# Optimization experiments

Measured on AMD Instinct MI355X. Metric: run time of the kernel, lower is better.

## Reference

```python
import jax, jax.numpy as jnp
import numpy as np
from jax import lax

N = 100_000          # points
NEIGH = 16           # max_num_neighbors
E = N * NEIGH        # edges
DIN = 128            # num_inputs
D2 = 64              # bottleneck dim = num_outputs // 4
DOUT = 256           # num_outputs
K = 15               # num_kernel_points
SIGMA = 0.04         # kernel_influence_dist = prev_grid_size * sigma
NEG = 0.1            # LeakyReLU slope
EPS = 1e-5           # BatchNorm eps


def leaky(x):
    return jnp.where(x >= 0, x, NEG * x)


def batchnorm(x, g, b):
    # training-mode BN over the point dimension (biased variance, like torch)
    m = jnp.mean(x, axis=0)
    v = jnp.var(x, axis=0)
    return (x - m) * (g / jnp.sqrt(v + EPS)) + b


def setup_inputs() -> dict:
    key = jax.random.key(0)
    ks = jax.random.split(key, 12)
    pos = jax.random.uniform(ks[0], (N, 4), dtype=jnp.float32) * 0.1  # col 0: batch idx (unused, non-strided)
    x = jax.random.normal(ks[1], (N, DIN), dtype=jnp.float32)
    e_ref = jax.random.randint(ks[2], (E,), 0, N)
    e_query = jax.random.randint(ks[3], (E,), 0, N)
    # fixed kernel point positions within the influence radius
    kernel_points = jax.random.normal(ks[4], (K, 3), dtype=jnp.float32) * (0.5 * SIGMA)
    W1 = jax.random.normal(ks[5], (DIN, D2), dtype=jnp.float32) / np.sqrt(DIN)
    W_kp = jax.random.normal(ks[6], (K, D2, D2), dtype=jnp.float32) / np.sqrt(D2 * K)
    W2 = jax.random.normal(ks[7], (D2, DOUT), dtype=jnp.float32) / np.sqrt(D2)
    Wsc = jax.random.normal(ks[8], (DIN, DOUT), dtype=jnp.float32) / np.sqrt(DIN)
    ones = lambda d: jnp.ones((d,), jnp.float32)
    zeros = lambda d: jnp.zeros((d,), jnp.float32)
    return dict(pos=pos, x=x, e_ref=e_ref, e_query=e_query,
                W1=W1, g1=ones(D2), b1=zeros(D2),
                kernel_points=kernel_points, W_kp=W_kp, gkp=ones(D2), bkp=zeros(D2),
                W2=W2, g2=ones(DOUT), b2=zeros(DOUT),
                Wsc=Wsc, gsc=ones(DOUT), bsc=zeros(DOUT))


def reference(pos, x, e_ref, e_query, W1, g1, b1, kernel_points, W_kp, gkp, bkp,
              W2, g2, b2, Wsc, gsc, bsc):
    n = x.shape[0]
    # bottleneck unary_1: Linear(no bias) -> BN -> LeakyReLU
    h = leaky(batchnorm(x @ W1, g1, b1))                      # [N, D2]
    # KPConv (rigid, linear influence, 'sum' aggregation); non-strided: query_pos == pos
    rel = pos[e_ref, 1:] - pos[e_query, 1:]                    # [E, 3]
    d2 = jnp.sum((rel[:, None, :] - kernel_points[None]) ** 2, axis=-1)  # [E, K]
    infl = jnp.maximum(0.0, 1.0 - jnp.sqrt(d2) / SIGMA)        # [E, K]
    feat_e = h[e_ref]                                          # [E, D2] neighbor gather

    def body(acc, inp):
        infl_k, Wk = inp                                       # [E], [D2, D2]
        agg = jax.ops.segment_sum(infl_k[:, None] * feat_e, e_query, num_segments=n)
        return acc + agg @ Wk, None

    y0 = jnp.zeros((n, W_kp.shape[-1]), x.dtype)
    y, _ = lax.scan(body, y0, (infl.T, W_kp))                  # [N, D2]
    # SimpleBlock post: BN -> LeakyReLU
    y = leaky(batchnorm(y, gkp, bkp))
    # bottleneck unary_2: Linear -> BN -> LeakyReLU
    y = leaky(batchnorm(y @ W2, g2, b2))
    # shortcut (num_inputs != num_outputs): Linear -> BN, no activation; residual add
    skip = batchnorm(x @ Wsc, gsc, bsc)
    return y + skip
```

## Files before the change

### kernel.cpp

```cpp
#include <hip/hip_runtime.h>
#include <math.h>

#define NP   100000
#define EDG  1600000
#define NK   15
#define SIGK 0.04f
#define SCH  2048
#define SNB  49
#define MAXE 256
#define AGP  968
#define ISTR 20

typedef __bf16 v8bf __attribute__((ext_vector_type(8)));
typedef __bf16 bf4  __attribute__((ext_vector_type(4)));
typedef float  v4f  __attribute__((ext_vector_type(4)));

__device__ __forceinline__ float lk(float v) { return v >= 0.f ? v : 0.1f * v; }
__device__ __forceinline__ float bf2f(__bf16 b) { return (float)b; }

template <int KIN, int NB, bool TRANS, bool OUTBF>
__global__ __launch_bounds__(256) void mgemm_k(const float* __restrict__ X,
                                               const __bf16* __restrict__ Wp,
                                               void* __restrict__ Out, int n, int Ntot,
                                               const float* __restrict__ ta,
                                               const float* __restrict__ tb,
                                               float* __restrict__ osum,
                                               float* __restrict__ osq) {
  constexpr int PITCH = KIN + 8;
  constexpr int NT = NB / 16;
  __shared__ __bf16 al[128 * PITCH];
  __shared__ float red[2][NB][4];
  const int tid = threadIdx.x;
  const int r0 = blockIdx.x << 7;
  const int nb0 = blockIdx.y * NB;

  constexpr int QKS = (KIN == 128) ? 5 : 4;
  for (int idx = tid; idx < (128 << QKS); idx += 256) {
    const int r = idx >> QKS, q = (idx & ((1 << QKS) - 1)) << 2;
    const int row = r0 + r;
    float4 v = make_float4(0.f, 0.f, 0.f, 0.f);
    if (row < n) {
      v = *(const float4*)&X[(size_t)row * KIN + q];
      if (TRANS) {
        v.x = lk(ta[q + 0] * v.x + tb[q + 0]);
        v.y = lk(ta[q + 1] * v.y + tb[q + 1]);
        v.z = lk(ta[q + 2] * v.z + tb[q + 2]);
        v.w = lk(ta[q + 3] * v.w + tb[q + 3]);
      }
    }
    bf4 o;
    o[0] = (__bf16)v.x; o[1] = (__bf16)v.y; o[2] = (__bf16)v.z; o[3] = (__bf16)v.w;
    *(bf4*)&al[r * PITCH + q] = o;
  }
  __syncthreads();

  const int wv = tid >> 6, lane = tid & 63;
  const int mr = lane & 15, quad = lane >> 4;
  const int ntg0 = nb0 >> 4;
  const int NTG = Ntot >> 4;
  v4f acc[2][NT];
#pragma unroll
  for (int a = 0; a < 2; ++a)
#pragma unroll
    for (int b = 0; b < NT; ++b) acc[a][b] = (v4f){0.f, 0.f, 0.f, 0.f};

#pragma unroll
  for (int ks = 0; ks < KIN / 32; ++ks) {
    v8bf bf[NT];
#pragma unroll
    for (int nt = 0; nt < NT; ++nt)
      bf[nt] = ((const v8bf*)Wp)[((size_t)ks * NTG + ntg0 + nt) * 64 + lane];
#pragma unroll
    for (int mt = 0; mt < 2; ++mt) {
      const int row = (wv << 5) + (mt << 4) + mr;
      const v8bf av = *(const v8bf*)&al[row * PITCH + (ks << 5) + (quad << 3)];
#pragma unroll
      for (int nt = 0; nt < NT; ++nt)
        acc[mt][nt] = __builtin_amdgcn_mfma_f32_16x16x32_bf16(av, bf[nt], acc[mt][nt], 0, 0, 0);
    }
  }

  float csum[NT], csq[NT];
#pragma unroll
  for (int nt = 0; nt < NT; ++nt) { csum[nt] = 0.f; csq[nt] = 0.f; }
#pragma unroll
  for (int mt = 0; mt < 2; ++mt)
#pragma unroll
    for (int nt = 0; nt < NT; ++nt)
#pragma unroll
      for (int r = 0; r < 4; ++r) {
        const float v = acc[mt][nt][r];
        const int row = r0 + (wv << 5) + (mt << 4) + (quad << 2) + r;
        if (row < n) {
          const size_t o = (size_t)row * Ntot + nb0 + (nt << 4) + mr;
          if (OUTBF) ((__bf16*)Out)[o] = (__bf16)v;
          else       ((float*)Out)[o] = v;
        }
        csum[nt] += v;
        csq[nt] += v * v;
      }
#pragma unroll
  for (int nt = 0; nt < NT; ++nt) {
    float s = csum[nt], q = csq[nt];
    s += __shfl_down(s, 32); s += __shfl_down(s, 16);
    q += __shfl_down(q, 32); q += __shfl_down(q, 16);
    if (quad == 0) { red[0][(nt << 4) + mr][wv] = s; red[1][(nt << 4) + mr][wv] = q; }
  }
  __syncthreads();
  if (tid < NB) {
    const float s = red[0][tid][0] + red[0][tid][1] + red[0][tid][2] + red[0][tid][3];
    const float q = red[1][tid][0] + red[1][tid][1] + red[1][tid][2] + red[1][tid][3];
    const int rep = (blockIdx.x & 31) * Ntot;
    atomicAdd(&osum[rep + nb0 + tid], s);
    atomicAdd(&osq[rep + nb0 + tid], q);
  }
}

__global__ void finalize_k(const float* __restrict__ sum, const float* __restrict__ sq,
                           const float* __restrict__ g, const float* __restrict__ b,
                           float* __restrict__ oa, float* __restrict__ ob, int C, int R,
                           float invn) {
  const int c = threadIdx.x;
  if (c < C) {
    float s = 0.f, q = 0.f;
    for (int r = 0; r < R; ++r) { s += sum[r * C + c]; q += sq[r * C + c]; }
    const float m = s * invn;
    const float var = q * invn - m * m;
    const float a = g[c] / sqrtf(var + 1e-5f);
    oa[c] = a;
    ob[c] = b[c] - m * a;
  }
}

__global__ __launch_bounds__(256) void final_k(float* __restrict__ o,
                                               const __bf16* __restrict__ t2,
                                               const __bf16* __restrict__ tsc,
                                               const float* __restrict__ a2,
                                               const float* __restrict__ b2,
                                               const float* __restrict__ asc,
                                               const float* __restrict__ bsc) {
  const int idx = (blockIdx.x << 8) + threadIdx.x;
  const int c = (idx << 2) & 255;
  const bf4 tv = *(const bf4*)&t2[(size_t)idx << 2];
  const bf4 sv = *(const bf4*)&tsc[(size_t)idx << 2];
  float4 r;
  r.x = lk(a2[c + 0] * bf2f(tv[0]) + b2[c + 0]) + asc[c + 0] * bf2f(sv[0]) + bsc[c + 0];
  r.y = lk(a2[c + 1] * bf2f(tv[1]) + b2[c + 1]) + asc[c + 1] * bf2f(sv[1]) + bsc[c + 1];
  r.z = lk(a2[c + 2] * bf2f(tv[2]) + b2[c + 2]) + asc[c + 2] * bf2f(sv[2]) + bsc[c + 2];
  r.w = lk(a2[c + 3] * bf2f(tv[3]) + b2[c + 3]) + asc[c + 3] * bf2f(sv[3]) + bsc[c + 3];
  ((float4*)o)[idx] = r;
}

__device__ __forceinline__ bool edge_active(const float* __restrict__ pos,
                                            const float* __restrict__ kp,
                                            int ref, int q) {
  const float4 pr = *(const float4*)&pos[ref * 4];
  const float4 pq = *(const float4*)&pos[q * 4];
  const float rx = pr.y - pq.y, ry = pr.z - pq.z, rz = pr.w - pq.w;
  bool act = false;
#pragma unroll
  for (int k = 0; k < NK; ++k) {
    const float dx = rx - kp[k * 3 + 0];
    const float dy = ry - kp[k * 3 + 1];
    const float dz = rz - kp[k * 3 + 2];
    act = act || (dx * dx + dy * dy + dz * dz < SIGK * SIGK);
  }
  return act;
}

__global__ __launch_bounds__(256) void hist_k(const int* __restrict__ er,
                                              const int* __restrict__ eq,
                                              const float* __restrict__ pos,
                                              const float* __restrict__ kp,
                                              int* __restrict__ cnt,
                                              unsigned char* __restrict__ flags) {
  const int stride = gridDim.x << 8;
  for (int e = (blockIdx.x << 8) + threadIdx.x; e < EDG; e += stride) {
    const int q = eq[e];
    const bool act = edge_active(pos, kp, er[e], q);
    flags[e] = act ? 1 : 0;
    if (act) atomicAdd(&cnt[q], 1);
  }
}

__global__ __launch_bounds__(256) void scanA_k(const int* __restrict__ cnt, int* __restrict__ part) {
  __shared__ int s[256];
  const int tid = threadIdx.x;
  const int base = blockIdx.x * SCH;
  int acc = 0;
  for (int i = tid; i < SCH; i += 256) {
    const int idx = base + i;
    if (idx < NP) acc += cnt[idx];
  }
  s[tid] = acc;
  __syncthreads();
  for (int d = 128; d > 0; d >>= 1) {
    if (tid < d) s[tid] += s[tid + d];
    __syncthreads();
  }
  if (tid == 0) part[blockIdx.x] = s[0];
}

__global__ void scanB_k(int* __restrict__ part, int* __restrict__ off) {
  if (threadIdx.x == 0) {
    int run = 0;
    for (int i = 0; i < SNB; ++i) { const int v = part[i]; part[i] = run; run += v; }
    off[NP] = run;
  }
}

__global__ __launch_bounds__(256) void scanC_k(const int* __restrict__ cnt,
                                               const int* __restrict__ part,
                                               int* __restrict__ off, int* __restrict__ cur) {
  __shared__ int s[256];
  const int tid = threadIdx.x;
  const int base = blockIdx.x * SCH + tid * 8;
  int loc[8];
  int mysum = 0;
#pragma unroll
  for (int j = 0; j < 8; ++j) {
    const int idx = base + j;
    const int v = (idx < NP) ? cnt[idx] : 0;
    loc[j] = mysum;
    mysum += v;
  }
  s[tid] = mysum;
  __syncthreads();
  for (int d = 1; d < 256; d <<= 1) {
    int v = (tid >= d) ? s[tid - d] : 0;
    __syncthreads();
    s[tid] += v;
    __syncthreads();
  }
  const int tb = part[blockIdx.x] + s[tid] - mysum;
#pragma unroll
  for (int j = 0; j < 8; ++j) {
    const int idx = base + j;
    if (idx < NP) { off[idx] = tb + loc[j]; cur[idx] = tb + loc[j]; }
  }
}

__global__ __launch_bounds__(256) void scat_k(const int* __restrict__ er,
                                              const int* __restrict__ eq,
                                              const unsigned char* __restrict__ flags,
                                              int* __restrict__ cur, int* __restrict__ sref) {
  const int stride = gridDim.x << 8;
  for (int e = (blockIdx.x << 8) + threadIdx.x; e < EDG; e += stride) {
    if (flags[e]) {
      const int p = atomicAdd(&cur[eq[e]], 1);
      if (p < EDG) sref[p] = er[e];
    }
  }
}

__device__ __forceinline__ void wshuf1(const float* W, __bf16* Wp, int idx, int Ntot) {
  const int j = idx & 7;
  const int lane = (idx >> 3) & 63;
  const int rest = idx >> 9;
  const int NTG = Ntot >> 4;
  const int ntg = rest % NTG;
  const int ks = rest / NTG;
  Wp[idx] = (__bf16)W[(size_t)(ks * 32 + ((lane >> 4) << 3) + j) * Ntot + ntg * 16 + (lane & 15)];
}

__global__ __launch_bounds__(256) void allshuf_k(const float* __restrict__ W1,
                                                 const float* __restrict__ Wsc,
                                                 const float* __restrict__ W2,
                                                 const float* __restrict__ Wkp,
                                                 __bf16* __restrict__ base) {
  const int i = (blockIdx.x << 8) + threadIdx.x;
  if (i < 8192) {
    wshuf1(W1, base, i, 64);
  } else if (i < 40960) {
    wshuf1(Wsc, base + 8192, i - 8192, 256);
  } else if (i < 57344) {
    wshuf1(W2, base + 40960, i - 40960, 256);
  } else if (i < 118784) {
    const int idx = i - 57344;
    const int j = idx & 7;
    const int lane = (idx >> 3) & 63;
    const int nt = (idx >> 9) & 3;
    const int kb = (idx >> 11) & 1;
    const int k = idx >> 12;
    const int kd = kb * 32 + ((lane >> 4) << 3) + j;
    const int n = nt * 16 + (lane & 15);
    (base + 57344)[idx] = (__bf16)Wkp[(k * 64 + kd) * 64 + n];
  }
}

__global__ __launch_bounds__(256, 4) void kpagg_k(const float* __restrict__ pos,
                                                  const int* __restrict__ sref,
                                                  const int* __restrict__ off,
                                                  const float* __restrict__ kpts,
                                                  const __bf16* __restrict__ Wf,
                                                  const __bf16* __restrict__ t1b,
                                                  const float* __restrict__ av,
                                                  const float* __restrict__ bv,
                                                  float* __restrict__ y,
                                                  float* __restrict__ osum,
                                                  float* __restrict__ osq) {
  constexpr int INFL_BYTES = MAXE * ISTR * 4;
  constexpr int UNION_BYTES = 16 * AGP * 2;
  __shared__ __align__(16) char uSm[UNION_BYTES];
  __shared__ int qoffL[17];
  __shared__ float kpL[48];
  __shared__ float4 qposL[16];
  __shared__ unsigned char qidxL[MAXE];
  float* inflF = (float*)uSm;
  int* refsL = (int*)(uSm + INFL_BYTES);
  __bf16* aggL = (__bf16*)uSm;

  const int tid = threadIdx.x;
  const int q0 = blockIdx.x << 4;
  if (tid < 17) qoffL[tid] = off[q0 + tid];
  if (tid >= 32 && tid < 77) kpL[tid - 32] = kpts[tid - 32];
  if (tid >= 80 && tid < 96) qposL[tid - 80] = *(const float4*)&pos[(q0 + tid - 80) * 4];
  __syncthreads();

  const int e0 = qoffL[0];
  int nE = qoffL[16] - e0;
  if (nE > MAXE) nE = MAXE;
  if (nE == 0 && tid == 0) refsL[0] = 0;

  if (tid < 16) {
    int a = qoffL[tid] - e0, b = qoffL[tid + 1] - e0;
    if (a > nE) a = nE;
    if (b > nE) b = nE;
    for (int i = a; i < b; ++i) qidxL[i] = (unsigned char)tid;
  }
  __syncthreads();

  if (tid < nE) {
    const int i = tid;
    const int ref = sref[e0 + i];
    refsL[i] = ref;
    const float4 pr = *(const float4*)&pos[ref * 4];
    const float4 pq = qposL[qidxL[i]];
    const float rx = pr.y - pq.y, ry = pr.z - pq.z, rz = pr.w - pq.w;
    float wk[16];
#pragma unroll
    for (int k = 0; k < NK; ++k) {
      const float dx = rx - kpL[k * 3 + 0];
      const float dy = ry - kpL[k * 3 + 1];
      const float dz = rz - kpL[k * 3 + 2];
      const float w = 1.f - sqrtf(dx * dx + dy * dy + dz * dz) * (1.f / SIGK);
      wk[k] = w > 0.f ? w : 0.f;
    }
    wk[15] = 0.f;
    *(float4*)&inflF[i * ISTR + 0]  = make_float4(wk[0], wk[1], wk[2], wk[3]);
    *(float4*)&inflF[i * ISTR + 4]  = make_float4(wk[4], wk[5], wk[6], wk[7]);
    *(float4*)&inflF[i * ISTR + 8]  = make_float4(wk[8], wk[9], wk[10], wk[11]);
    *(float4*)&inflF[i * ISTR + 12] = make_float4(wk[12], wk[13], wk[14], wk[15]);
  }
  __syncthreads();

  const int wv = tid >> 6, lane = tid & 63;
  const int ql = (wv << 2) + (lane >> 4);
  const int t4 = (lane & 15) << 2;
  const int le0 = qoffL[ql] - e0;
  int le1 = qoffL[ql + 1] - e0;
  if (le1 > nE) le1 = nE;
  const int len = le1 - le0;

  const float4 aV = *(const float4*)&av[t4];
  const float4 bV = *(const float4*)&bv[t4];

  float acc[NK][4];
#pragma unroll
  for (int k = 0; k < NK; ++k) { acc[k][0] = acc[k][1] = acc[k][2] = acc[k][3] = 0.f; }

  const int j0 = (len > 0) ? le0 : 0;
  const int j1 = (len > 1) ? le0 + 1 : j0;
  const int j2 = (len > 2) ? le0 + 2 : j1;
  bf4 hA = *(const bf4*)&t1b[(size_t)refsL[j0] * 64 + t4];
  bf4 hB = *(const bf4*)&t1b[(size_t)refsL[j1] * 64 + t4];
  int refC = refsL[j2];
#pragma unroll 2
  for (int j = le0; j < le1; ++j) {
    const bf4 hv = hA;
    hA = hB;
    hB = *(const bf4*)&t1b[(size_t)refC * 64 + t4];
    const int jn = (j + 3 < le1) ? j + 3 : le1 - 1;
    refC = refsL[jn];
    const float f0 = lk(aV.x * bf2f(hv[0]) + bV.x);
    const float f1 = lk(aV.y * bf2f(hv[1]) + bV.y);
    const float f2 = lk(aV.z * bf2f(hv[2]) + bV.z);
    const float f3 = lk(aV.w * bf2f(hv[3]) + bV.w);
    const float4 wA = *(const float4*)&inflF[j * ISTR + 0];
    const float4 wB = *(const float4*)&inflF[j * ISTR + 4];
    const float4 wC = *(const float4*)&inflF[j * ISTR + 8];
    const float4 wD = *(const float4*)&inflF[j * ISTR + 12];
    const float wk[NK] = {wA.x, wA.y, wA.z, wA.w, wB.x, wB.y, wB.z, wB.w,
                          wC.x, wC.y, wC.z, wC.w, wD.x, wD.y, wD.z};
#pragma unroll
    for (int k = 0; k < NK; ++k) {
      acc[k][0] += wk[k] * f0;
      acc[k][1] += wk[k] * f1;
      acc[k][2] += wk[k] * f2;
      acc[k][3] += wk[k] * f3;
    }
  }

  __syncthreads();

#pragma unroll
  for (int k = 0; k < NK; ++k) {
    bf4 o;
    o[0] = (__bf16)acc[k][0]; o[1] = (__bf16)acc[k][1];
    o[2] = (__bf16)acc[k][2]; o[3] = (__bf16)acc[k][3];
    *(bf4*)&aggL[ql * AGP + k * 64 + t4] = o;
  }
  __syncthreads();

  const int m = lane & 15, quad = lane >> 4;
  v4f yacc = {0.f, 0.f, 0.f, 0.f};
  const v8bf* Wf8 = (const v8bf*)Wf;
#pragma unroll
  for (int k = 0; k < NK; ++k)
#pragma unroll
    for (int kb = 0; kb < 2; ++kb) {
      const v8bf av2 = *(const v8bf*)&aggL[m * AGP + k * 64 + kb * 32 + (quad << 3)];
      const v8bf bv2 = Wf8[((k * 2 + kb) * 4 + wv) * 64 + lane];
      yacc = __builtin_amdgcn_mfma_f32_16x16x32_bf16(av2, bv2, yacc, 0, 0, 0);
    }

  float s = 0.f, q2 = 0.f;
#pragma unroll
  for (int r = 0; r < 4; ++r) {
    const float v = yacc[r];
    y[(size_t)(q0 + (quad << 2) + r) * 64 + (wv << 4) + m] = v;
    s += v; q2 += v * v;
  }
  s += __shfl_down(s, 32); s += __shfl_down(s, 16);
  q2 += __shfl_down(q2, 32); q2 += __shfl_down(q2, 16);
  if (quad == 0) {
    const int rep = (blockIdx.x & 63) << 6;
    atomicAdd(&osum[rep + (wv << 4) + m], s);
    atomicAdd(&osq[rep + (wv << 4) + m], q2);
  }
}

extern "C" void kernel_launch(void* const* d_in, const int* in_sizes, int n_in,
                              void* d_out, int out_size, void* d_ws, size_t ws_size,
                              hipStream_t stream) {
  const float* pos = (const float*)d_in[0];
  const float* x   = (const float*)d_in[1];
  const int* er    = (const int*)d_in[2];
  const int* eq    = (const int*)d_in[3];
  const float* W1  = (const float*)d_in[4];
  const float* g1  = (const float*)d_in[5];
  const float* b1  = (const float*)d_in[6];
  const float* kp  = (const float*)d_in[7];
  const float* Wkp = (const float*)d_in[8];
  const float* gkp = (const float*)d_in[9];
  const float* bkp = (const float*)d_in[10];
  const float* W2  = (const float*)d_in[11];
  const float* g2  = (const float*)d_in[12];
  const float* b2  = (const float*)d_in[13];
  const float* Wsc = (const float*)d_in[14];
  const float* gsc = (const float*)d_in[15];
  const float* bsc = (const float*)d_in[16];
  float* out = (float*)d_out;
  float* ws = (float*)d_ws;

  float* sum1 = ws;
  float* sq1  = ws + 2048;
  float* sumsc = ws + 4096;
  float* sqsc  = ws + 12288;
  float* sumy = ws + 20480;
  float* sqy  = ws + 24576;
  float* sum2 = ws + 28672;
  float* sq2  = ws + 36864;
  float* a1v = ws + 45056;   float* b1v  = ws + 45120;
  float* ascv = ws + 45184;  float* bscv = ws + 45440;
  float* ayv = ws + 45696;   float* byv  = ws + 45760;
  float* a2v = ws + 45824;   float* b2v  = ws + 46080;

  __bf16* Wpb = (__bf16*)(ws + 49152);
  __bf16* W1p = Wpb;
  __bf16* Wscp = Wpb + 8192;
  __bf16* W2p = Wpb + 40960;
  __bf16* Wfp = Wpb + 57344;
  float* ybuf = ws + 114688 + 3200000;
  float* t1bf = ybuf + 6400000;
  __bf16* t1b = (__bf16*)t1bf;
  __bf16* tscb = (__bf16*)ybuf;
  int* cnt = (int*)(t1bf + 6400000);
  int* off = cnt + 100352;
  int* cur = off + 100352;
  int* part = cur + 100352;
  int* sref = part + 256;
  unsigned char* flags = (unsigned char*)(sref + EDG);
  __bf16* t2b = (__bf16*)cnt;

  const float invn = 1.f / (float)NP;

  (void)hipMemsetAsync(ws, 0, 49152 * sizeof(float), stream);
  (void)hipMemsetAsync(cnt, 0, 100352 * sizeof(int), stream);

  allshuf_k<<<464, 256, 0, stream>>>(W1, Wsc, W2, Wkp, Wpb);

  mgemm_k<128, 64, false, true><<<dim3(782, 1), 256, 0, stream>>>(
      x, W1p, t1b, NP, 64, nullptr, nullptr, sum1, sq1);
  finalize_k<<<1, 256, 0, stream>>>(sum1, sq1, g1, b1, a1v, b1v, 64, 32, invn);

  hist_k<<<2048, 256, 0, stream>>>(er, eq, pos, kp, cnt, flags);
  scanA_k<<<SNB, 256, 0, stream>>>(cnt, part);
  scanB_k<<<1, 64, 0, stream>>>(part, off);
  scanC_k<<<SNB, 256, 0, stream>>>(cnt, part, off, cur);
  scat_k<<<2048, 256, 0, stream>>>(er, eq, flags, cur, sref);

  kpagg_k<<<6250, 256, 0, stream>>>(pos, sref, off, kp, Wfp, t1b, a1v, b1v,
                                    ybuf, sumy, sqy);
  finalize_k<<<1, 256, 0, stream>>>(sumy, sqy, gkp, bkp, ayv, byv, 64, 64, invn);

  mgemm_k<64, 128, true, true><<<dim3(782, 2), 256, 0, stream>>>(
      ybuf, W2p, t2b, NP, 256, ayv, byv, sum2, sq2);
  finalize_k<<<1, 256, 0, stream>>>(sum2, sq2, g2, b2, a2v, b2v, 256, 32, invn);

  mgemm_k<128, 128, false, true><<<dim3(782, 2), 256, 0, stream>>>(
      x, Wscp, tscb, NP, 256, nullptr, nullptr, sumsc, sqsc);
  finalize_k<<<1, 256, 0, stream>>>(sumsc, sqsc, gsc, bsc, ascv, bscv, 256, 32, invn);

  final_k<<<25000, 256, 0, stream>>>(out, t2b, tscb, a2v, b2v, ascv, bscv);
}
```

Measured before the change: 526.2 us.

## Stage neighbor features into LDS cooperatively before KPConv aggregation loop

Neighbor feature rows are now gathered by all 256 threads into a shared-memory tile before aggregation, with the BN-affine and LeakyReLU applied once per edge during staging. The per-query loop then reads preprocessed bf16 features from LDS instead of issuing dependent global gathers through a manual software prefetch. This raises shared-memory use (infl + refs + feature tile), so the launch-bounds occupancy hint drops from 4 to 2 blocks per CU. It also adds a bf16 rounding of the activated features and an extra barrier.

```diff
diff --git a/kernel.cpp b/kernel.cpp
--- a/kernel.cpp
+++ b/kernel.cpp
@@ -10,6 +10,7 @@
 #define MAXE 256
 #define AGP  968
 #define ISTR 20
+#define HLP  68
 
 typedef __bf16 v8bf __attribute__((ext_vector_type(8)));
 typedef __bf16 bf4  __attribute__((ext_vector_type(4)));
@@ -288,7 +289,7 @@
   }
 }
 
-__global__ __launch_bounds__(256, 4) void kpagg_k(const float* __restrict__ pos,
+__global__ __launch_bounds__(256, 2) void kpagg_k(const float* __restrict__ pos,
                                                   const int* __restrict__ sref,
                                                   const int* __restrict__ off,
                                                   const float* __restrict__ kpts,
@@ -300,14 +301,18 @@
                                                   float* __restrict__ osum,
                                                   float* __restrict__ osq) {
   constexpr int INFL_BYTES = MAXE * ISTR * 4;
-  constexpr int UNION_BYTES = 16 * AGP * 2;
+  constexpr int REFS_BYTES = MAXE * 4;
+  constexpr int HL_BYTES = MAXE * HLP * 2;
+  constexpr int UNION_BYTES = INFL_BYTES + REFS_BYTES + HL_BYTES;
   __shared__ __align__(16) char uSm[UNION_BYTES];
   __shared__ int qoffL[17];
   __shared__ float kpL[48];
   __shared__ float4 qposL[16];
   __shared__ unsigned char qidxL[MAXE];
+  __shared__ float abL[128];
   float* inflF = (float*)uSm;
   int* refsL = (int*)(uSm + INFL_BYTES);
+  __bf16* hL = (__bf16*)(uSm + INFL_BYTES + REFS_BYTES);
   __bf16* aggL = (__bf16*)uSm;
 
   const int tid = threadIdx.x;
@@ -315,12 +320,13 @@
   if (tid < 17) qoffL[tid] = off[q0 + tid];
   if (tid >= 32 && tid < 77) kpL[tid - 32] = kpts[tid - 32];
   if (tid >= 80 && tid < 96) qposL[tid - 80] = *(const float4*)&pos[(q0 + tid - 80) * 4];
+  if (tid >= 128 && tid < 192) abL[tid - 128] = av[tid - 128];
+  if (tid >= 192 && tid < 256) abL[tid - 128] = bv[tid - 192];
   __syncthreads();
 
   const int e0 = qoffL[0];
   int nE = qoffL[16] - e0;
   if (nE > MAXE) nE = MAXE;
-  if (nE == 0 && tid == 0) refsL[0] = 0;
 
   if (tid < 16) {
     int a = qoffL[tid] - e0, b = qoffL[tid + 1] - e0;
@@ -354,38 +360,38 @@
   }
   __syncthreads();
 
+  const int nCh = nE << 4;
+#pragma unroll 2
+  for (int c = tid; c < nCh; c += 256) {
+    const int i = c >> 4;
+    const int t4c = (c & 15) << 2;
+    const bf4 v = *(const bf4*)&t1b[(size_t)refsL[i] * 64 + t4c];
+    const float4 aV = *(const float4*)&abL[t4c];
+    const float4 bV = *(const float4*)&abL[64 + t4c];
+    bf4 o;
+    o[0] = (__bf16)lk(aV.x * bf2f(v[0]) + bV.x);
+    o[1] = (__bf16)lk(aV.y * bf2f(v[1]) + bV.y);
+    o[2] = (__bf16)lk(aV.z * bf2f(v[2]) + bV.z);
+    o[3] = (__bf16)lk(aV.w * bf2f(v[3]) + bV.w);
+    *(bf4*)&hL[i * HLP + t4c] = o;
+  }
+  __syncthreads();
+
   const int wv = tid >> 6, lane = tid & 63;
   const int ql = (wv << 2) + (lane >> 4);
   const int t4 = (lane & 15) << 2;
   const int le0 = qoffL[ql] - e0;
   int le1 = qoffL[ql + 1] - e0;
   if (le1 > nE) le1 = nE;
-  const int len = le1 - le0;
-
-  const float4 aV = *(const float4*)&av[t4];
-  const float4 bV = *(const float4*)&bv[t4];
 
   float acc[NK][4];
 #pragma unroll
   for (int k = 0; k < NK; ++k) { acc[k][0] = acc[k][1] = acc[k][2] = acc[k][3] = 0.f; }
 
-  const int j0 = (len > 0) ? le0 : 0;
-  const int j1 = (len > 1) ? le0 + 1 : j0;
-  const int j2 = (len > 2) ? le0 + 2 : j1;
-  bf4 hA = *(const bf4*)&t1b[(size_t)refsL[j0] * 64 + t4];
-  bf4 hB = *(const bf4*)&t1b[(size_t)refsL[j1] * 64 + t4];
-  int refC = refsL[j2];
 #pragma unroll 2
   for (int j = le0; j < le1; ++j) {
-    const bf4 hv = hA;
-    hA = hB;
-    hB = *(const bf4*)&t1b[(size_t)refC * 64 + t4];
-    const int jn = (j + 3 < le1) ? j + 3 : le1 - 1;
-    refC = refsL[jn];
-    const float f0 = lk(aV.x * bf2f(hv[0]) + bV.x);
-    const float f1 = lk(aV.y * bf2f(hv[1]) + bV.y);
-    const float f2 = lk(aV.z * bf2f(hv[2]) + bV.z);
-    const float f3 = lk(aV.w * bf2f(hv[3]) + bV.w);
+    const bf4 hv = *(const bf4*)&hL[j * HLP + t4];
+    const float f0 = bf2f(hv[0]), f1 = bf2f(hv[1]), f2 = bf2f(hv[2]), f3 = bf2f(hv[3]);
     const float4 wA = *(const float4*)&inflF[j * ISTR + 0];
     const float4 wB = *(const float4*)&inflF[j * ISTR + 4];
     const float4 wC = *(const float4*)&inflF[j * ISTR + 8];
```

Result: slower. 572.5 us (+8.8%).

## Precompute normalized features and halve KPConv shared buffer to raise occupancy

Applied to the files above, without the earlier changes.

A new elementwise pass applies the first BatchNorm and LeakyReLU to the bottleneck features once per point, so the KPConv aggregation kernel no longer redoes that per edge. The aggregation kernel's shared-memory aggregate buffer is split into two halves processed in turn, which shrinks LDS use. Launch bounds rise from 4 to 7 blocks per CU and the edge loop unroll is reduced to ease register pressure. The cost is an extra kernel launch with a read and write of the feature array, plus an extra barrier pair.

```diff
diff --git a/kernel.cpp b/kernel.cpp
--- a/kernel.cpp
+++ b/kernel.cpp
@@ -8,8 +8,8 @@
 #define SCH  2048
 #define SNB  49
 #define MAXE 256
-#define AGP  968
 #define ISTR 20
+#define AGPH 520
 
 typedef __bf16 v8bf __attribute__((ext_vector_type(8)));
 typedef __bf16 bf4  __attribute__((ext_vector_type(4)));
@@ -130,6 +130,21 @@
     oa[c] = a;
     ob[c] = b[c] - m * a;
   }
+}
+
+__global__ __launch_bounds__(256) void normleaky_k(const __bf16* __restrict__ t,
+                                                   __bf16* __restrict__ hb,
+                                                   const float* __restrict__ a,
+                                                   const float* __restrict__ b) {
+  const int idx = (blockIdx.x << 8) + threadIdx.x;
+  const int c = (idx << 2) & 63;
+  const bf4 v = *(const bf4*)&t[(size_t)idx << 2];
+  bf4 o;
+  o[0] = (__bf16)lk(a[c + 0] * bf2f(v[0]) + b[c + 0]);
+  o[1] = (__bf16)lk(a[c + 1] * bf2f(v[1]) + b[c + 1]);
+  o[2] = (__bf16)lk(a[c + 2] * bf2f(v[2]) + b[c + 2]);
+  o[3] = (__bf16)lk(a[c + 3] * bf2f(v[3]) + b[c + 3]);
+  *(bf4*)&hb[(size_t)idx << 2] = o;
 }
 
 __global__ __launch_bounds__(256) void final_k(float* __restrict__ o,
@@ -288,19 +303,20 @@
   }
 }
 
-__global__ __launch_bounds__(256, 4) void kpagg_k(const float* __restrict__ pos,
+__global__ __launch_bounds__(256, 7) void kpagg_k(const float* __restrict__ pos,
                                                   const int* __restrict__ sref,
                                                   const int* __restrict__ off,
                                                   const float* __restrict__ kpts,
                                                   const __bf16* __restrict__ Wf,
-                                                  const __bf16* __restrict__ t1b,
-                                                  const float* __restrict__ av,
-                                                  const float* __restrict__ bv,
+                                                  const __bf16* __restrict__ hb,
                                                   float* __restrict__ y,
                                                   float* __restrict__ osum,
                                                   float* __restrict__ osq) {
   constexpr int INFL_BYTES = MAXE * ISTR * 4;
-  constexpr int UNION_BYTES = 16 * AGP * 2;
+  constexpr int REFS_BYTES = MAXE * 4;
+  constexpr int AGG_BYTES = 16 * AGPH * 2;
+  constexpr int UNION_BYTES = (INFL_BYTES + REFS_BYTES > AGG_BYTES)
+                                  ? (INFL_BYTES + REFS_BYTES) : AGG_BYTES;
   __shared__ __align__(16) char uSm[UNION_BYTES];
   __shared__ int qoffL[17];
   __shared__ float kpL[48];
@@ -308,7 +324,7 @@
   __shared__ unsigned char qidxL[MAXE];
   float* inflF = (float*)uSm;
   int* refsL = (int*)(uSm + INFL_BYTES);
-  __bf16* aggL = (__bf16*)uSm;
+  __bf16* aggH = (__bf16*)uSm;
 
   const int tid = threadIdx.x;
   const int q0 = blockIdx.x << 4;
@@ -362,9 +378,6 @@
   if (le1 > nE) le1 = nE;
   const int len = le1 - le0;
 
-  const float4 aV = *(const float4*)&av[t4];
-  const float4 bV = *(const float4*)&bv[t4];
-
   float acc[NK][4];
 #pragma unroll
   for (int k = 0; k < NK; ++k) { acc[k][0] = acc[k][1] = acc[k][2] = acc[k][3] = 0.f; }
@@ -372,20 +385,17 @@
   const int j0 = (len > 0) ? le0 : 0;
   const int j1 = (len > 1) ? le0 + 1 : j0;
   const int j2 = (len > 2) ? le0 + 2 : j1;
-  bf4 hA = *(const bf4*)&t1b[(size_t)refsL[j0] * 64 + t4];
-  bf4 hB = *(const bf4*)&t1b[(size_t)refsL[j1] * 64 + t4];
+  bf4 hA = *(const bf4*)&hb[(size_t)refsL[j0] * 64 + t4];
+  bf4 hB = *(const bf4*)&hb[(size_t)refsL[j1] * 64 + t4];
   int refC = refsL[j2];
-#pragma unroll 2
+#pragma unroll 1
   for (int j = le0; j < le1; ++j) {
     const bf4 hv = hA;
     hA = hB;
-    hB = *(const bf4*)&t1b[(size_t)refC * 64 + t4];
+    hB = *(const bf4*)&hb[(size_t)refC * 64 + t4];
     const int jn = (j + 3 < le1) ? j + 3 : le1 - 1;
     refC = refsL[jn];
-    const float f0 = lk(aV.x * bf2f(hv[0]) + bV.x);
-    const float f1 = lk(aV.y * bf2f(hv[1]) + bV.y);
-    const float f2 = lk(aV.z * bf2f(hv[2]) + bV.z);
-    const float f3 = lk(aV.w * bf2f(hv[3]) + bV.w);
+    const float f0 = bf2f(hv[0]), f1 = bf2f(hv[1]), f2 = bf2f(hv[2]), f3 = bf2f(hv[3]);
     const float4 wA = *(const float4*)&inflF[j * ISTR + 0];
     const float4 wB = *(const float4*)&inflF[j * ISTR + 4];
     const float4 wC = *(const float4*)&inflF[j * ISTR + 8];
@@ -401,28 +411,31 @@
     }
   }
 
-  __syncthreads();
-
-#pragma unroll
-  for (int k = 0; k < NK; ++k) {
-    bf4 o;
-    o[0] = (__bf16)acc[k][0]; o[1] = (__bf16)acc[k][1];
-    o[2] = (__bf16)acc[k][2]; o[3] = (__bf16)acc[k][3];
-    *(bf4*)&aggL[ql * AGP + k * 64 + t4] = o;
-  }
-  __syncthreads();
-
   const int m = lane & 15, quad = lane >> 4;
   v4f yacc = {0.f, 0.f, 0.f, 0.f};
   const v8bf* Wf8 = (const v8bf*)Wf;
 #pragma unroll
-  for (int k = 0; k < NK; ++k)
-#pragma unroll
-    for (int kb = 0; kb < 2; ++kb) {
-      const v8bf av2 = *(const v8bf*)&aggL[m * AGP + k * 64 + kb * 32 + (quad << 3)];
-      const v8bf bv2 = Wf8[((k * 2 + kb) * 4 + wv) * 64 + lane];
-      yacc = __builtin_amdgcn_mfma_f32_16x16x32_bf16(av2, bv2, yacc, 0, 0, 0);
+  for (int half = 0; half < 2; ++half) {
+    const int k0h = half << 3;
+    const int kn = half ? 7 : 8;
+    __syncthreads();
+#pragma unroll
+    for (int k = 0; k < kn; ++k) {
+      bf4 o;
+      o[0] = (__bf16)acc[k0h + k][0]; o[1] = (__bf16)acc[k0h + k][1];
+      o[2] = (__bf16)acc[k0h + k][2]; o[3] = (__bf16)acc[k0h + k][3];
+      *(bf4*)&aggH[ql * AGPH + k * 64 + t4] = o;
     }
+    __syncthreads();
+#pragma unroll
+    for (int k = 0; k < kn; ++k)
+#pragma unroll
+      for (int kb = 0; kb < 2; ++kb) {
+        const v8bf av2 = *(const v8bf*)&aggH[m * AGPH + k * 64 + kb * 32 + (quad << 3)];
+        const v8bf bv2 = Wf8[(((k0h + k) * 2 + kb) * 4 + wv) * 64 + lane];
+        yacc = __builtin_amdgcn_mfma_f32_16x16x32_bf16(av2, bv2, yacc, 0, 0, 0);
+      }
+  }
 
   float s = 0.f, q2 = 0.f;
 #pragma unroll
@@ -481,6 +494,7 @@
   __bf16* Wscp = Wpb + 8192;
   __bf16* W2p = Wpb + 40960;
   __bf16* Wfp = Wpb + 57344;
+  __bf16* hb = (__bf16*)(ws + 114688);
   float* ybuf = ws + 114688 + 3200000;
   float* t1bf = ybuf + 6400000;
   __bf16* t1b = (__bf16*)t1bf;
@@ -503,6 +517,7 @@
   mgemm_k<128, 64, false, true><<<dim3(782, 1), 256, 0, stream>>>(
       x, W1p, t1b, NP, 64, nullptr, nullptr, sum1, sq1);
   finalize_k<<<1, 256, 0, stream>>>(sum1, sq1, g1, b1, a1v, b1v, 64, 32, invn);
+  normleaky_k<<<6250, 256, 0, stream>>>(t1b, hb, a1v, b1v);
 
   hist_k<<<2048, 256, 0, stream>>>(er, eq, pos, kp, cnt, flags);
   scanA_k<<<SNB, 256, 0, stream>>>(cnt, part);
@@ -510,8 +525,7 @@
   scanC_k<<<SNB, 256, 0, stream>>>(cnt, part, off, cur);
   scat_k<<<2048, 256, 0, stream>>>(er, eq, flags, cur, sref);
 
-  kpagg_k<<<6250, 256, 0, stream>>>(pos, sref, off, kp, Wfp, t1b, a1v, b1v,
-                                    ybuf, sumy, sqy);
+  kpagg_k<<<6250, 256, 0, stream>>>(pos, sref, off, kp, Wfp, hb, ybuf, sumy, sqy);
   finalize_k<<<1, 256, 0, stream>>>(sumy, sqy, gkp, bkp, ayv, byv, 64, 64, invn);
 
   mgemm_k<64, 128, true, true><<<dim3(782, 2), 256, 0, stream>>>(
```

Result: slower. 630.8 us (+19.9%).
